# Optimization experiments

Hardware: AMD Instinct MI355X
Metric: run time of the kernel (lower is better)

Reference implementation:

```python
import jax, jax.numpy as jnp
import numpy as np

D_MODEL = 512
N_HEADS = 8
D_FF = 1024
LV = 2048
LT = 512
GAMMA = 0.9
SCALE_BASE = 512  # XPOS default scale_base


def _dup_interleave(m):
    # (L, d/2) -> (L, d) duplicating each column: [a,b] -> [a,a,b,b]
    return jnp.repeat(m, 2, axis=-1)


def _xpos(x, downscale=False):
    # XPOS rotary embedding (RetNet-style), x: (B, L, d)
    B, L, d = x.shape
    half = d // 2
    s = (jnp.arange(0, d, 2, dtype=jnp.float32) + 0.4 * d) / (1.4 * d)  # (d/2,)
    scale = s[None, :] ** (jnp.arange(L, dtype=jnp.float32)[:, None] / SCALE_BASE)  # (L, d/2)
    inv_freq = 1.0 / (10000.0 ** (jnp.arange(half, dtype=jnp.float32) / half))
    ang = jnp.arange(L, dtype=jnp.float32)[:, None] * inv_freq[None, :]  # (L, d/2)
    if downscale:
        scale = 1.0 / scale
    sin = _dup_interleave(jnp.sin(ang) * scale)[None]  # (1, L, d)
    cos = _dup_interleave(jnp.cos(ang) * scale)[None]
    x1, x2 = x[..., 0::2], x[..., 1::2]
    rot = jnp.stack((-x2, x1), axis=-1).reshape(x.shape)  # rotate_every_two
    return x * cos + rot * sin


def _sine_pos(L, d):
    # DETR-style normalized 1D sine position embedding, mask = ones(1, L)
    x_embed = jnp.arange(1, L + 1, dtype=jnp.float32)  # cumsum of ones
    x_embed = x_embed / (x_embed[-1] + 1e-6) * (2.0 * np.pi)
    dim_t = jnp.arange(d, dtype=jnp.float32)
    dim_t = 10000.0 ** (2.0 * jnp.floor(dim_t / 2.0) / d)
    pos = x_embed[:, None] / dim_t[None, :]  # (L, d)
    pos = jnp.stack((jnp.sin(pos[:, 0::2]), jnp.cos(pos[:, 1::2])), axis=2).reshape(L, d)
    return pos[None]  # (1, L, d)


def _ln(x, w, b, eps=1e-5):
    mu = jnp.mean(x, axis=-1, keepdims=True)
    var = jnp.var(x, axis=-1, keepdims=True)
    return (x - mu) / jnp.sqrt(var + eps) * w + b


def _ret_forward(src_vid, src_txt, ln1_w, ln1_b, wq, bq, wk, bk, wv, bv, wo, bo,
                 lin1_w, lin1_b, lin2_w, lin2_b, ln2_w, ln2_b, ln3_w, ln3_b,
                 learn_ret_w):
    B, Lv, D = src_vid.shape
    Lt = src_txt.shape[1]
    h, dk = N_HEADS, D // N_HEADS

    # retention decay matrix D[n,m] = gamma^(n-m) for n>=m else 0
    n = jnp.arange(Lv)
    delta = jnp.maximum(n[:, None] - n[None, :], 0).astype(jnp.float32)
    Dm = jnp.where(n[:, None] >= n[None, :], GAMMA ** delta, 0.0)

    # learned sparse mask
    learn = jax.nn.sigmoid(learn_ret_w.reshape(Lv, Lv))
    diag = jnp.eye(Lv, dtype=jnp.float32)
    video_ret = (1.0 - diag) * learn
    learn_mask = diag + video_ret
    mask = Dm * learn_mask  # mask_choice == 'both'
    loss_sparsity = jnp.mean(jnp.abs(video_ret))

    # position encodings
    pos_vid_q = _xpos(src_vid)
    pos_vid_k = _xpos(src_vid, downscale=True)
    pos_txt = _sine_pos(Lt, D)
    src = jnp.concatenate([src_vid, src_txt], axis=1)       # (B, Lv+Lt, D)
    pos = jnp.concatenate([pos_vid_q, pos_txt], axis=1)
    pos_k = jnp.concatenate([pos_vid_k, pos_txt], axis=1)

    # --- RetLayer (eval mode: dropout = identity) ---
    src2 = _ln(src, ln1_w, ln1_b)
    q = src2[:, :Lv] + pos[:, :Lv]
    k = src2[:, :Lv] + pos_k[:, :Lv]
    v = src2[:, :Lv]

    # multi-head attention with MULTIPLICATIVE mask on logits
    qh = (q @ wq.T + bq).reshape(B, Lv, h, dk) / jnp.sqrt(jnp.float32(dk))
    kh = (k @ wk.T + bk).reshape(B, Lv, h, dk)
    vh = (v @ wv.T + bv).reshape(B, Lv, h, dk)
    attn = jnp.einsum('blhd,bmhd->bhlm', qh, kh) * mask[None, None]
    attn = jax.nn.softmax(attn, axis=-1)
    vid_att = jnp.einsum('bhlm,bmhd->blhd', attn, vh).reshape(B, Lv, D)
    vid_att = vid_att @ wo.T + bo

    src2 = jnp.concatenate([vid_att, src2[:, Lv:]], axis=1) + pos
    src = src + src2
    src2 = _ln(src, ln2_w, ln2_b)
    src2 = jax.nn.gelu(src2 @ lin1_w.T + lin1_b, approximate=False) @ lin2_w.T + lin2_b
    src = src + src2
    src = _ln(src, ln3_w, ln3_b)
    return src[:, :Lv], src[:, Lv:], loss_sparsity


def setup_inputs() -> dict:
    key = jax.random.key(0)
    ks = jax.random.split(key, 12)
    D, F = D_MODEL, D_FF
    w = lambda k, shp: (jax.random.normal(k, shp, dtype=jnp.float32) * 0.02)
    return {
        'src_vid': jax.random.normal(ks[0], (1, LV, D), dtype=jnp.float32),
        'src_txt': jax.random.normal(ks[1], (1, LT, D), dtype=jnp.float32),
        'ln1_w': jnp.ones((D,), jnp.float32), 'ln1_b': jnp.zeros((D,), jnp.float32),
        'wq': w(ks[2], (D, D)), 'bq': jnp.zeros((D,), jnp.float32),
        'wk': w(ks[3], (D, D)), 'bk': jnp.zeros((D,), jnp.float32),
        'wv': w(ks[4], (D, D)), 'bv': jnp.zeros((D,), jnp.float32),
        'wo': w(ks[5], (D, D)), 'bo': jnp.zeros((D,), jnp.float32),
        'lin1_w': w(ks[6], (F, D)), 'lin1_b': jnp.zeros((F,), jnp.float32),
        'lin2_w': w(ks[7], (D, F)), 'lin2_b': jnp.zeros((D,), jnp.float32),
        'ln2_w': jnp.ones((D,), jnp.float32), 'ln2_b': jnp.zeros((D,), jnp.float32),
        'ln3_w': jnp.ones((D,), jnp.float32), 'ln3_b': jnp.zeros((D,), jnp.float32),
        'learn_ret_w': jax.random.normal(ks[8], (LV * LV,), dtype=jnp.float32),
    }


def reference(src_vid, src_txt, ln1_w, ln1_b, wq, bq, wk, bk, wv, bv, wo, bo,
              lin1_w, lin1_b, lin2_w, lin2_b, ln2_w, ln2_b, ln3_w, ln3_b,
              learn_ret_w):
    return _ret_forward(src_vid, src_txt, ln1_w, ln1_b, wq, bq, wk, bk, wv, bv,
                        wo, bo, lin1_w, lin1_b, lin2_w, lin2_b, ln2_w, ln2_b,
                        ln3_w, ln3_b, learn_ret_w)
```

## Files before the change

kernel.cpp:

```cpp
#include <hip/hip_runtime.h>
#include <hip/hip_bf16.h>
#include <math.h>

#define LVID 2048
#define LTXT 512
#define DMOD 512
#define LTOT 2560
#define LOG2_GAMMA (-0.15200309344504995f)
#define LOG2E 1.4426950408889634f

typedef __bf16 bf16x8 __attribute__((ext_vector_type(8)));
typedef float f32x4 __attribute__((ext_vector_type(4)));

__device__ inline f32x4 mfma_bf16(bf16x8 a, bf16x8 b, f32x4 c) {
  return __builtin_amdgcn_mfma_f32_16x16x32_bf16(a, b, c, 0, 0, 0);
}

__device__ inline void gload_lds16(const void* g, void* l) {
  __builtin_amdgcn_global_load_lds(
      (const __attribute__((address_space(1))) void*)g,
      (__attribute__((address_space(3))) void*)l, 16, 0, 0);
}

union U8 { __hip_bfloat16 b[8]; uint4 u; };

__global__ __launch_bounds__(256) void k_prep_ln1(
    const float* __restrict__ lw, float* __restrict__ premask2,
    float* __restrict__ lossp, float* __restrict__ vts,
    const float* __restrict__ wq, const float* __restrict__ wk,
    const float* __restrict__ wv, const float* __restrict__ wo,
    const float* __restrict__ l1, const float* __restrict__ l2,
    __hip_bfloat16* __restrict__ dst,
    const float* __restrict__ src_vid, const float* __restrict__ src_txt,
    const float* __restrict__ w, const float* __restrict__ b,
    __hip_bfloat16* __restrict__ acat, float* __restrict__ srcA,
    float* __restrict__ posb) {
  int tid = threadIdx.x;
  int blk = blockIdx.x;
  if (blk < 64) vts[blk * 256 + tid] = 0.f;
  if (blk < 2048) {
    __shared__ float red[256];
    int i = blk;
    int i0r = i & ~63;
    int tloCol = (i0r > 900) ? (((i0r - 900) >> 6) << 6) : 0;
    int idx0 = (blk * 256 + tid) * 8;
    int j0 = idx0 & 2047;
    float4 lv0 = *(const float4*)&lw[idx0];
    float4 lv1 = *(const float4*)&lw[idx0 + 4];
    float lvv[8] = {lv0.x, lv0.y, lv0.z, lv0.w, lv1.x, lv1.y, lv1.z, lv1.w};
    float pm[8];
    float s = 0.f;
#pragma unroll
    for (int e = 0; e < 8; e++) {
      int j = j0 + e;
      float sig = 1.f / (1.f + __expf(-lvv[e]));
      if (j != i) s += sig;
      float m = (j > i) ? 0.f
              : ((j == i) ? 1.f : exp2f((float)(i - j) * LOG2_GAMMA) * sig);
      pm[e] = m * LOG2E;
    }
    if (j0 >= tloCol && j0 < i0r + 64) {
      *(float4*)&premask2[idx0]     = *(float4*)&pm[0];
      *(float4*)&premask2[idx0 + 4] = *(float4*)&pm[4];
    }
    red[tid] = s; __syncthreads();
    for (int st = 128; st > 0; st >>= 1) { if (tid < st) red[tid] += red[tid + st]; __syncthreads(); }
    if (tid == 0) lossp[blk] = red[0];
  } else if (blk < 4096) {
    int i4 = (blk - 2048) * 256 + tid;
    const float* sp; int base;
    if (i4 < 131072)      { if (i4 < 65536)  { sp = wq; base = 0; }      else { sp = wk; base = 65536; } }
    else if (i4 < 262144) { if (i4 < 196608) { sp = wv; base = 131072; } else { sp = wo; base = 196608; } }
    else if (i4 < 393216) { sp = l1; base = 262144; }
    else                  { sp = l2; base = 393216; }
    float4 v = ((const float4*)sp)[i4 - base];
    __hip_bfloat16 o[4] = {__float2bfloat16(v.x), __float2bfloat16(v.y),
                           __float2bfloat16(v.z), __float2bfloat16(v.w)};
    *(uint2*)(dst + (size_t)i4 * 4) = *(uint2*)o;
  } else {
    int row = (blk - 4096) * 4 + (tid >> 6);
    int lane = tid & 63;
    const float* xs = (row < LVID) ? (src_vid + (size_t)row * DMOD)
                                   : (src_txt + (size_t)(row - LVID) * DMOD);
    float x[8];
    { float4 v0 = *(const float4*)&xs[lane * 8];
      float4 v1 = *(const float4*)&xs[lane * 8 + 4];
      x[0]=v0.x; x[1]=v0.y; x[2]=v0.z; x[3]=v0.w;
      x[4]=v1.x; x[5]=v1.y; x[6]=v1.z; x[7]=v1.w; }
    float s = 0.f;
#pragma unroll
    for (int i = 0; i < 8; i++) s += x[i];
#pragma unroll
    for (int st = 1; st < 64; st <<= 1) s += __shfl_xor(s, st, 64);
    float mu = s * (1.f / DMOD);
    float vs = 0.f;
#pragma unroll
    for (int i = 0; i < 8; i++) { float d = x[i] - mu; vs += d * d; }
#pragma unroll
    for (int st = 1; st < 64; st <<= 1) vs += __shfl_xor(vs, st, 64);
    float inv = rsqrtf(vs * (1.f / DMOD) + 1e-5f);
    float y[8];
    { float4 w0 = *(const float4*)&w[lane * 8];
      float4 w1 = *(const float4*)&w[lane * 8 + 4];
      float4 b0 = *(const float4*)&b[lane * 8];
      float4 b1 = *(const float4*)&b[lane * 8 + 4];
      float wv_[8] = {w0.x,w0.y,w0.z,w0.w,w1.x,w1.y,w1.z,w1.w};
      float bv_[8] = {b0.x,b0.y,b0.z,b0.w,b1.x,b1.y,b1.z,b1.w};
#pragma unroll
      for (int i = 0; i < 8; i++) y[i] = (x[i] - mu) * inv * wv_[i] + bv_[i]; }
    size_t base = (size_t)row * DMOD + lane * 8;
    if (row < LVID) {
      U8 pv;
#pragma unroll
      for (int i = 0; i < 8; i++) pv.b[i] = __float2bfloat16(y[i]);
      *(uint4*)&acat[(size_t)(4096 + row) * DMOD + lane * 8] = pv.u;
      float pq[8], pk[8];
      float l = (float)row;
#pragma unroll
      for (int p = 0; p < 4; p++) {
        int j = lane * 4 + p;
        float sj = (2.f * j + 204.8f) * (1.f / 716.8f);
        float scale = __powf(sj, l * (1.f / 512.f));
        float invfreq = __powf(10000.f, -(float)j * (1.f / 256.f));
        float sn, cs; __sincosf(l * invfreq, &sn, &cs);
        float cq = cs * scale, sq = sn * scale;
        pq[2*p]   = x[2*p] * cq - x[2*p+1] * sq;
        pq[2*p+1] = x[2*p+1] * cq + x[2*p] * sq;
        float isc = 1.f / scale;
        float ck = cs * isc, sk = sn * isc;
        pk[2*p]   = x[2*p] * ck - x[2*p+1] * sk;
        pk[2*p+1] = x[2*p+1] * ck + x[2*p] * sk;
      }
      *(float4*)&posb[base]     = *(float4*)&pq[0];
      *(float4*)&posb[base + 4] = *(float4*)&pq[4];
      U8 pqv, pkv;
#pragma unroll
      for (int i = 0; i < 8; i++) {
        pqv.b[i] = __float2bfloat16(y[i] + pq[i]);
        pkv.b[i] = __float2bfloat16(y[i] + pk[i]);
      }
      *(uint4*)&acat[(size_t)row * DMOD + lane * 8] = pqv.u;
      *(uint4*)&acat[(size_t)(2048 + row) * DMOD + lane * 8] = pkv.u;
    } else {
      int l = row - LVID;
      float xe = (float)(l + 1) * (6.28318530717958647692f / 512.000001f);
      float o8[8];
#pragma unroll
      for (int p = 0; p < 4; p++) {
        int j = lane * 4 + p;
        float dimt = __powf(10000.f, (float)j * (1.f / 256.f));
        float a = xe / dimt;
        o8[2*p]   = x[2*p]   + y[2*p]   + __sinf(a);
        o8[2*p+1] = x[2*p+1] + y[2*p+1] + __cosf(a);
      }
      *(float4*)&srcA[base]     = *(float4*)&o8[0];
      *(float4*)&srcA[base + 4] = *(float4*)&o8[4];
    }
  }
}

__global__ __launch_bounds__(256) void k_ln2(
    const float* __restrict__ srcA,
    const float* __restrict__ w, const float* __restrict__ b,
    __hip_bfloat16* __restrict__ obf) {
  int row = blockIdx.x * 4 + (threadIdx.x >> 6);
  int lane = threadIdx.x & 63;
  size_t base = (size_t)row * DMOD + lane * 8;
  float x[8];
  { float4 v0 = *(const float4*)&srcA[base];
    float4 v1 = *(const float4*)&srcA[base + 4];
    x[0]=v0.x; x[1]=v0.y; x[2]=v0.z; x[3]=v0.w;
    x[4]=v1.x; x[5]=v1.y; x[6]=v1.z; x[7]=v1.w; }
  float s = 0.f;
#pragma unroll
  for (int i = 0; i < 8; i++) s += x[i];
#pragma unroll
  for (int st = 1; st < 64; st <<= 1) s += __shfl_xor(s, st, 64);
  float mu = s * (1.f / DMOD);
  float vs = 0.f;
#pragma unroll
  for (int i = 0; i < 8; i++) { float d = x[i] - mu; vs += d * d; }
#pragma unroll
  for (int st = 1; st < 64; st <<= 1) vs += __shfl_xor(vs, st, 64);
  float inv = rsqrtf(vs * (1.f / DMOD) + 1e-5f);
  float4 w0 = *(const float4*)&w[lane * 8];
  float4 w1 = *(const float4*)&w[lane * 8 + 4];
  float4 b0 = *(const float4*)&b[lane * 8];
  float4 b1 = *(const float4*)&b[lane * 8 + 4];
  float wv_[8] = {w0.x,w0.y,w0.z,w0.w,w1.x,w1.y,w1.z,w1.w};
  float bv_[8] = {b0.x,b0.y,b0.z,b0.w,b1.x,b1.y,b1.z,b1.w};
  U8 o;
#pragma unroll
  for (int i = 0; i < 8; i++)
    o.b[i] = __float2bfloat16((x[i] - mu) * inv * wv_[i] + bv_[i]);
  *(uint4*)&obf[base] = o.u;
}

__global__ __launch_bounds__(256) void k_ln3(
    const float* __restrict__ srcA, const float* __restrict__ ffo0,
    const float* __restrict__ ffo1,
    const float* __restrict__ w, const float* __restrict__ b,
    float* __restrict__ o, const float* __restrict__ lossp) {
  if (blockIdx.x == 0 && threadIdx.x < 64) {
    float s = 0.f;
    for (int i = threadIdx.x; i < 2048; i += 64) s += lossp[i];
#pragma unroll
    for (int st = 1; st < 64; st <<= 1) s += __shfl_xor(s, st, 64);
    if (threadIdx.x == 0) o[1310720] = s * (1.f / 4194304.f);
  }
  int row = blockIdx.x * 4 + (threadIdx.x >> 6);
  int lane = threadIdx.x & 63;
  size_t base = (size_t)row * DMOD + lane * 8;
  float x[8];
  { float4 a0 = *(const float4*)&srcA[base];
    float4 a1 = *(const float4*)&srcA[base + 4];
    float4 f0 = *(const float4*)&ffo0[base];
    float4 f1 = *(const float4*)&ffo0[base + 4];
    float4 g0 = *(const float4*)&ffo1[base];
    float4 g1 = *(const float4*)&ffo1[base + 4];
    x[0]=a0.x+f0.x+g0.x; x[1]=a0.y+f0.y+g0.y; x[2]=a0.z+f0.z+g0.z; x[3]=a0.w+f0.w+g0.w;
    x[4]=a1.x+f1.x+g1.x; x[5]=a1.y+f1.y+g1.y; x[6]=a1.z+f1.z+g1.z; x[7]=a1.w+f1.w+g1.w; }
  float s = 0.f;
#pragma unroll
  for (int i = 0; i < 8; i++) s += x[i];
#pragma unroll
  for (int st = 1; st < 64; st <<= 1) s += __shfl_xor(s, st, 64);
  float mu = s * (1.f / DMOD);
  float vs = 0.f;
#pragma unroll
  for (int i = 0; i < 8; i++) { float d = x[i] - mu; vs += d * d; }
#pragma unroll
  for (int st = 1; st < 64; st <<= 1) vs += __shfl_xor(vs, st, 64);
  float inv = rsqrtf(vs * (1.f / DMOD) + 1e-5f);
  float4 w0 = *(const float4*)&w[lane * 8];
  float4 w1 = *(const float4*)&w[lane * 8 + 4];
  float4 b0 = *(const float4*)&b[lane * 8];
  float4 b1 = *(const float4*)&b[lane * 8 + 4];
  float wv_[8] = {w0.x,w0.y,w0.z,w0.w,w1.x,w1.y,w1.z,w1.w};
  float bv_[8] = {b0.x,b0.y,b0.z,b0.w,b1.x,b1.y,b1.z,b1.w};
  float y[8];
#pragma unroll
  for (int i = 0; i < 8; i++) y[i] = (x[i] - mu) * inv * wv_[i] + bv_[i];
  *(float4*)&o[base]     = *(float4*)&y[0];
  *(float4*)&o[base + 4] = *(float4*)&y[4];
}

template <int EPI>
__global__ __launch_bounds__(256) void k_gemm5(
    const __hip_bfloat16* __restrict__ A, const __hip_bfloat16* __restrict__ W0,
    const float* __restrict__ b0, const float* __restrict__ b1,
    const float* __restrict__ b2, void* __restrict__ Cv,
    const float* __restrict__ res1, const float* __restrict__ res2,
    __hip_bfloat16* __restrict__ vT, float* __restrict__ vts,
    int M, int N, int K) {
  __shared__ __hip_bfloat16 sA[2][4096];
  __shared__ __hip_bfloat16 sB[2][4096];
  int tid = threadIdx.x, lane = tid & 63, w = tid >> 6;
  int c16 = lane & 15, q4 = lane >> 4;
  int bm = blockIdx.y * 64, bn = blockIdx.x * 64;
  int seg = (EPI == 3) ? (bm >> 11) : 0;
  const __hip_bfloat16* Wp = (EPI == 3) ? (W0 + (size_t)seg * ((size_t)N * K)) : W0;
  int kb   = (EPI == 5) ? (int)blockIdx.z * (K >> 1) : 0;
  int Keff = (EPI == 5) ? (K >> 1) : K;
  int r0 = tid >> 2, cc0 = (tid & 3) * 8;
  const __hip_bfloat16* gA = A  + (size_t)(bm + r0) * K + kb + cc0;
  const __hip_bfloat16* gB = Wp + (size_t)(bn + r0) * K + kb + cc0;
  auto stage = [&](int buf, int k0) {
    gload_lds16(gA + k0,      &sA[buf][(size_t)tid * 8]);
    gload_lds16(gA + k0 + 32, &sA[buf][2048 + (size_t)tid * 8]);
    gload_lds16(gB + k0,      &sB[buf][(size_t)tid * 8]);
    gload_lds16(gB + k0 + 32, &sB[buf][2048 + (size_t)tid * 8]);
  };
  f32x4 acc[2][2];
  { f32x4 z = {0.f,0.f,0.f,0.f}; acc[0][0]=z; acc[0][1]=z; acc[1][0]=z; acc[1][1]=z; }
  int wm = w & 1, wn = w >> 1;
  const int S = Keff >> 6;
  stage(0, 0);
  for (int s = 0; s < S; s++) {
    __syncthreads();
    if (s + 1 < S) stage((s + 1) & 1, (s + 1) * 64);
    int bf = s & 1;
#pragma unroll
    for (int kc = 0; kc < 2; kc++) {
      bf16x8 a0  = *(const bf16x8*)&sA[bf][kc*2048 + (wm*32 + c16) * 32 + q4*8];
      bf16x8 a1  = *(const bf16x8*)&sA[bf][kc*2048 + (wm*32 + 16 + c16) * 32 + q4*8];
      bf16x8 bv0 = *(const bf16x8*)&sB[bf][kc*2048 + (wn*32 + c16) * 32 + q4*8];
      bf16x8 bv1 = *(const bf16x8*)&sB[bf][kc*2048 + (wn*32 + 16 + c16) * 32 + q4*8];
      acc[0][0] = mfma_bf16(a0, bv0, acc[0][0]);
      acc[0][1] = mfma_bf16(a0, bv1, acc[0][1]);
      acc[1][0] = mfma_bf16(a1, bv0, acc[1][0]);
      acc[1][1] = mfma_bf16(a1, bv1, acc[1][1]);
    }
  }
  float alpha = (EPI == 3 && seg == 0) ? 0.125f : 1.f;
  const float* bp = (EPI == 3) ? (seg == 0 ? b0 : (seg == 1 ? b1 : b2)) : b0;
  if (EPI == 3 && seg == 2) {
    int tile = (bm & 2047) >> 6;
    float vsum[2] = {0.f, 0.f};
#pragma unroll
    for (int j = 0; j < 2; j++) {
      int n = bn + wn*32 + j*16 + c16;
      float bs = bp[n];
#pragma unroll
      for (int i = 0; i < 2; i++) {
        ushort4 u; float vv[4];
#pragma unroll
        for (int r = 0; r < 4; r++) {
          __hip_bfloat16 vb = __float2bfloat16(acc[i][j][r] + bs);
          ((__hip_bfloat16*)&u)[r] = vb;
          vv[r] = __bfloat162float(vb);
        }
        int jj = (bm & 2047) + wm*32 + i*16 + q4*4;
        *(ushort4*)&vT[(size_t)n * 2048 + jj] = u;
        vsum[j] += vv[0] + vv[1] + vv[2] + vv[3];
      }
    }
#pragma unroll
    for (int j = 0; j < 2; j++) {
      float s2 = vsum[j];
      s2 += __shfl_xor(s2, 16, 64);
      s2 += __shfl_xor(s2, 32, 64);
      int n = bn + wn*32 + j*16 + c16;
      if (q4 == 0) atomicAdd(&vts[(size_t)(n >> 6) * 2048 + tile * 64 + (n & 63)], s2);
    }
    return;
  }
#pragma unroll
  for (int j = 0; j < 2; j++) {
    int n = bn + wn*32 + j*16 + c16;
    float bs = bp[n];
    if (EPI == 5 && blockIdx.z != 0) bs = 0.f;
#pragma unroll
    for (int i = 0; i < 2; i++) {
#pragma unroll
      for (int r = 0; r < 4; r++) {
        int m = bm + wm*32 + i*16 + q4*4 + r;
        float v = (acc[i][j][r] + bs) * alpha;
        if (EPI == 4) v = 0.5f * v * (1.f + erff(v * 0.70710678118654752f));
        if (EPI == 2) {
          size_t off = (size_t)m * N + n;
          ((float*)Cv)[off] = v + res1[off] + res2[off];
        } else if (EPI == 4) {
          ((__hip_bfloat16*)Cv)[(size_t)m * N + n] = __float2bfloat16(v);
        } else if (EPI == 5) {
          ((float*)Cv)[(size_t)blockIdx.z * 1310720 + (size_t)m * N + n] = v;
        } else {
          ((__hip_bfloat16*)Cv)[(size_t)(m & 2047) * 1024 + seg * 512 + n] = __float2bfloat16(v);
        }
      }
    }
  }
}

__global__ __launch_bounds__(256) void k_attn(
    const __hip_bfloat16* __restrict__ qkb,
    const float* __restrict__ premask2,
    const __hip_bfloat16* __restrict__ vT,
    __hip_bfloat16* __restrict__ Obuf,
    float* __restrict__ ml) {
  __shared__ __hip_bfloat16 sQ[64][72];
  __shared__ __hip_bfloat16 sK[2][64][72];
  __shared__ __hip_bfloat16 sVt[2][64][72];
  __shared__ __hip_bfloat16 sP[64][72];
  int i0 = blockIdx.x * 64, h = blockIdx.y, z = blockIdx.z;
  int tid = threadIdx.x, lane = tid & 63, w = tid >> 6;
  int c16 = lane & 15, q4 = lane >> 4;
  {
    int r = tid >> 2, c0 = (tid & 3) * 16;
    const __hip_bfloat16* g = qkb + (size_t)(i0 + r) * 1024 + h * 64 + c0;
    *(uint4*)&sQ[r][c0]     = *(const uint4*)g;
    *(uint4*)&sQ[r][c0 + 8] = *(const uint4*)(g + 8);
  }
  int thi = i0 >> 6;
  int tlo = (i0 > 900) ? ((i0 - 900) >> 6) : 0;
  int nt_ = thi - tlo + 1;
  int t0 = tlo + ((nt_ * z) >> 2);
  int t1 = tlo + ((nt_ * (z + 1)) >> 2) - 1;
  float rm = 0.f, rz = 0.f;
  f32x4 O[4];
  { f32x4 zz = {0.f,0.f,0.f,0.f}; O[0]=zz; O[1]=zz; O[2]=zz; O[3]=zz; }
  int kr = tid >> 2, kc = (tid & 3) * 16;
  uint4 pk0, pk1, pv0, pv1;
  if (t0 <= t1) {
    const __hip_bfloat16* gk = qkb + (size_t)(t0*64 + kr) * 1024 + 512 + h*64 + kc;
    pk0 = *(const uint4*)gk; pk1 = *(const uint4*)(gk + 8);
    const __hip_bfloat16* gv = vT + (size_t)(h*64 + kr) * 2048 + t0*64 + kc;
    pv0 = *(const uint4*)gv; pv1 = *(const uint4*)(gv + 8);
  }
  for (int t = t0; t <= t1; t++) {
    int buf = (t - t0) & 1;
    *(uint4*)&sK[buf][kr][kc]      = pk0;
    *(uint4*)&sK[buf][kr][kc + 8]  = pk1;
    *(uint4*)&sVt[buf][kr][kc]     = pv0;
    *(uint4*)&sVt[buf][kr][kc + 8] = pv1;
    __syncthreads();
    if (t < t1) {
      const __hip_bfloat16* gk = qkb + (size_t)((t+1)*64 + kr) * 1024 + 512 + h*64 + kc;
      pk0 = *(const uint4*)gk; pk1 = *(const uint4*)(gk + 8);
      const __hip_bfloat16* gv = vT + (size_t)(h*64 + kr) * 2048 + (t+1)*64 + kc;
      pv0 = *(const uint4*)gv; pv1 = *(const uint4*)(gv + 8);
    }
    bf16x8 bq0 = *(const bf16x8*)&sQ[w*16 + c16][q4*8];
    bf16x8 bq1 = *(const bf16x8*)&sQ[w*16 + c16][32 + q4*8];
    f32x4 St[4];
#pragma unroll
    for (int jt = 0; jt < 4; jt++) {
      f32x4 zz = {0.f,0.f,0.f,0.f};
      bf16x8 a0 = *(const bf16x8*)&sK[buf][jt*16 + c16][q4*8];
      bf16x8 a1 = *(const bf16x8*)&sK[buf][jt*16 + c16][32 + q4*8];
      zz = mfma_bf16(a0, bq0, zz);
      zz = mfma_bf16(a1, bq1, zz);
      St[jt] = zz;
    }
    int qg = i0 + w*16 + c16;
    float lg[4][4];
    float tmax = -3.0e38f;
#pragma unroll
    for (int jt = 0; jt < 4; jt++) {
      float4 pm = *(const float4*)&premask2[(size_t)qg * 2048 + t*64 + jt*16 + q4*4];
      lg[jt][0] = St[jt][0] * pm.x; lg[jt][1] = St[jt][1] * pm.y;
      lg[jt][2] = St[jt][2] * pm.z; lg[jt][3] = St[jt][3] * pm.w;
#pragma unroll
      for (int r = 0; r < 4; r++) tmax = fmaxf(tmax, lg[jt][r]);
    }
    tmax = fmaxf(tmax, __shfl_xor(tmax, 16, 64));
    tmax = fmaxf(tmax, __shfl_xor(tmax, 32, 64));
    float mn = fmaxf(rm, tmax);
    float al = exp2f(rm - mn);
    rm = mn;
    float zp = 0.f;
#pragma unroll
    for (int jt = 0; jt < 4; jt++) {
      U8 e4;
      float e0 = exp2f(lg[jt][0] - rm), e1 = exp2f(lg[jt][1] - rm);
      float e2 = exp2f(lg[jt][2] - rm), e3 = exp2f(lg[jt][3] - rm);
      zp += e0 + e1 + e2 + e3;
      e4.b[0] = __float2bfloat16(e0); e4.b[1] = __float2bfloat16(e1);
      e4.b[2] = __float2bfloat16(e2); e4.b[3] = __float2bfloat16(e3);
      *(uint2*)&sP[w*16 + c16][jt*16 + q4*4] = *(uint2*)&e4.b[0];
    }
    zp += __shfl_xor(zp, 16, 64);
    zp += __shfl_xor(zp, 32, 64);
    rz = rz * al + zp;
    float alr[4];
#pragma unroll
    for (int r = 0; r < 4; r++) alr[r] = __shfl(al, q4*4 + r, 64);
#pragma unroll
    for (int dt = 0; dt < 4; dt++)
#pragma unroll
      for (int r = 0; r < 4; r++) O[dt][r] *= alr[r];
    bf16x8 ap0 = *(const bf16x8*)&sP[w*16 + c16][q4*8];
    bf16x8 ap1 = *(const bf16x8*)&sP[w*16 + c16][32 + q4*8];
#pragma unroll
    for (int dt = 0; dt < 4; dt++) {
      bf16x8 bv0 = *(const bf16x8*)&sVt[buf][dt*16 + c16][q4*8];
      bf16x8 bv1 = *(const bf16x8*)&sVt[buf][dt*16 + c16][32 + q4*8];
      O[dt] = mfma_bf16(ap0, bv0, O[dt]);
      O[dt] = mfma_bf16(ap1, bv1, O[dt]);
    }
  }
  __hip_bfloat16* ob = Obuf + (size_t)z * (2048 * 512);
#pragma unroll
  for (int dt = 0; dt < 4; dt++) {
    int d = dt*16 + c16;
#pragma unroll
    for (int r = 0; r < 4; r++)
      ob[(size_t)(i0 + w*16 + q4*4 + r) * DMOD + h*64 + d] = __float2bfloat16(O[dt][r]);
  }
  if (q4 == 0) {
    size_t mi = (((size_t)z * 8 + h) * 2048 + i0 + w*16 + c16) * 2;
    ml[mi] = rm; ml[mi + 1] = rz;
  }
}

__global__ __launch_bounds__(256) void k_comb(
    const __hip_bfloat16* __restrict__ Obuf, const float* __restrict__ ml,
    const float* __restrict__ vts,
    __hip_bfloat16* __restrict__ outp) {
  __shared__ float sV[32][64];
  __shared__ float sS[64];
  __shared__ float sC[64][6];
  int i0 = blockIdx.x * 64, h = blockIdx.y;
  int tid = threadIdx.x;
  int thi = i0 >> 6;
  int tlo = (i0 > 900) ? ((i0 - 900) >> 6) : 0;
  int n = thi - tlo + 1;
  float nu = (float)(2048 - 64 * n);
  {
    const float4* src = (const float4*)(vts + (size_t)h * 2048);
    ((float4*)&sV[0][0])[tid * 2]     = src[tid * 2];
    ((float4*)&sV[0][0])[tid * 2 + 1] = src[tid * 2 + 1];
  }
  __syncthreads();
  if (tid < 64) {
    float s = 0.f;
    for (int t = 0; t < 32; t++) if (t < tlo || t > thi) s += sV[t][tid];
    sS[tid] = s;
  } else if (tid < 128) {
    int r = tid - 64;
    int row = i0 + r;
    float m[4], l[4];
#pragma unroll
    for (int z = 0; z < 4; z++) {
      size_t mi = (((size_t)z * 8 + h) * 2048 + row) * 2;
      m[z] = ml[mi]; l[z] = ml[mi + 1];
    }
    float M = fmaxf(fmaxf(m[0], m[1]), fmaxf(m[2], m[3]));
    float au = exp2f(-M);
    float a[4], D = nu * au;
#pragma unroll
    for (int z = 0; z < 4; z++) { a[z] = exp2f(m[z] - M); D += l[z] * a[z]; }
    float dinv = 1.f / D;
#pragma unroll
    for (int z = 0; z < 4; z++) sC[r][z] = a[z] * dinv;
    sC[r][4] = au * dinv;
  }
  __syncthreads();
  int r = tid >> 2, dc = (tid & 3) * 16;
  size_t off = (size_t)(i0 + r) * DMOD + h * 64 + dc;
  float c[4];
#pragma unroll
  for (int z = 0; z < 4; z++) c[z] = sC[r][z];
  float cu = sC[r][4];
  float va[16], vb[16];
#pragma unroll
  for (int k = 0; k < 16; k++) { va[k] = sS[dc + (k & 7)] * 0.f; }
  U8 oa, obb;
#pragma unroll
  for (int k = 0; k < 8; k++) { va[k] = sS[dc + k] * cu; vb[k] = sS[dc + 8 + k] * cu; }
#pragma unroll
  for (int z = 0; z < 4; z++) {
    U8 pa, pb;
    pa.u = *(const uint4*)&Obuf[(size_t)z * 2048 * 512 + off];
    pb.u = *(const uint4*)&Obuf[(size_t)z * 2048 * 512 + off + 8];
#pragma unroll
    for (int k = 0; k < 8; k++) {
      va[k] += __bfloat162float(pa.b[k]) * c[z];
      vb[k] += __bfloat162float(pb.b[k]) * c[z];
    }
  }
#pragma unroll
  for (int k = 0; k < 8; k++) {
    oa.b[k]  = __float2bfloat16(va[k]);
    obb.b[k] = __float2bfloat16(vb[k]);
  }
  *(uint4*)&outp[off]     = oa.u;
  *(uint4*)&outp[off + 8] = obb.u;
}

extern "C" void kernel_launch(void* const* d_in, const int* in_sizes, int n_in,
                              void* d_out, int out_size, void* d_ws, size_t ws_size,
                              hipStream_t stream) {
  const float* src_vid = (const float*)d_in[0];
  const float* src_txt = (const float*)d_in[1];
  const float* ln1_w = (const float*)d_in[2];
  const float* ln1_b = (const float*)d_in[3];
  const float* wq = (const float*)d_in[4];
  const float* bq = (const float*)d_in[5];
  const float* wk = (const float*)d_in[6];
  const float* bk = (const float*)d_in[7];
  const float* wv = (const float*)d_in[8];
  const float* bv = (const float*)d_in[9];
  const float* wo = (const float*)d_in[10];
  const float* bo = (const float*)d_in[11];
  const float* lin1_w = (const float*)d_in[12];
  const float* lin1_b = (const float*)d_in[13];
  const float* lin2_w = (const float*)d_in[14];
  const float* lin2_b = (const float*)d_in[15];
  const float* ln2_w = (const float*)d_in[16];
  const float* ln2_b = (const float*)d_in[17];
  const float* ln3_w = (const float*)d_in[18];
  const float* ln3_b = (const float*)d_in[19];
  const float* lw = (const float*)d_in[20];
  float* out = (float*)d_out;

  const size_t MB = 1048576;
  char* wsb = (char*)d_ws;
  float* premask2       = (float*)(wsb + 0);
  __hip_bfloat16* wqb   = (__hip_bfloat16*)(wsb + 16*MB);
  __hip_bfloat16* wob   = wqb + 786432;
  __hip_bfloat16* l1b   = wqb + 1048576;
  __hip_bfloat16* l2b   = wqb + 1572864;
  __hip_bfloat16* acat  = (__hip_bfloat16*)(wsb + 20*MB);
  __hip_bfloat16* qkb   = (__hip_bfloat16*)(wsb + 26*MB);
  __hip_bfloat16* vTb   = (__hip_bfloat16*)(wsb + 30*MB);
  __hip_bfloat16* Obuf  = (__hip_bfloat16*)(wsb + 32*MB);
  float* mlb            = (float*)(wsb + 40*MB);
  float* vts            = (float*)(wsb + 41*MB);
  __hip_bfloat16* vattb = (__hip_bfloat16*)(wsb + 42*MB);
  float* srcA           = (float*)(wsb + 44*MB);
  float* posb           = (float*)(wsb + 49*MB);
  __hip_bfloat16* s2b   = (__hip_bfloat16*)(wsb + 54*MB);
  __hip_bfloat16* hidb  = (__hip_bfloat16*)(wsb + 57*MB);
  float* ffo0           = (float*)(wsb + 62*MB);
  float* ffo1           = (float*)(wsb + 67*MB);
  float* lossp          = (float*)(wsb + 72*MB);

  k_prep_ln1<<<4736, 256, 0, stream>>>(lw, premask2, lossp, vts,
      wq, wk, wv, wo, lin1_w, lin2_w, wqb,
      src_vid, src_txt, ln1_w, ln1_b, acat, srcA, posb);

  k_gemm5<3><<<dim3(8, 96), 256, 0, stream>>>(acat, wqb, bq, bk, bv,
      qkb, nullptr, nullptr, vTb, vts, 6144, 512, 512);
  k_attn<<<dim3(32, 8, 4), 256, 0, stream>>>(qkb, premask2, vTb, Obuf, mlb);
  k_comb<<<dim3(32, 8), 256, 0, stream>>>(Obuf, mlb, vts, vattb);
  k_gemm5<2><<<dim3(8, 32), 256, 0, stream>>>(vattb, wob, bo, nullptr, nullptr,
      srcA, src_vid, posb, nullptr, nullptr, 2048, 512, 512);
  k_ln2<<<640, 256, 0, stream>>>(srcA, ln2_w, ln2_b, s2b);
  k_gemm5<4><<<dim3(16, 40), 256, 0, stream>>>(s2b, l1b, lin1_b, nullptr, nullptr,
      hidb, nullptr, nullptr, nullptr, nullptr, 2560, 1024, 512);
  k_gemm5<5><<<dim3(8, 40, 2), 256, 0, stream>>>(hidb, l2b, lin2_b, nullptr, nullptr,
      ffo0, nullptr, nullptr, nullptr, nullptr, 2560, 512, 1024);
  k_ln3<<<640, 256, 0, stream>>>(srcA, ffo0, ffo1, ln3_w, ln3_b, out, lossp);
}
```

Baseline: 206.6 us.

## Compute decay mask inline in attention and use 128-row GEMM tiles

The precomputed premask buffer is removed. The attention kernel now computes gamma decay times sigmoid of the learned weights directly from the raw weights, and the prep kernel only reduces the sigmoid sum for the loss using fewer, wider blocks. Separately, a new GEMM variant with 128x64 tiles (4x2 MFMA per wave) is used for the QKV, FFN1 and FFN2 GEMMs to increase data reuse. This saves a 16MB write and read pass for the mask, at the cost of extra exp and sigmoid work inside attention and fewer GEMM blocks per launch.

```diff
diff --git a/kernel.cpp b/kernel.cpp
--- a/kernel.cpp
+++ b/kernel.cpp
@@ -25,8 +25,8 @@
 union U8 { __hip_bfloat16 b[8]; uint4 u; };
 
 __global__ __launch_bounds__(256) void k_prep_ln1(
-    const float* __restrict__ lw, float* __restrict__ premask2,
-    float* __restrict__ lossp, float* __restrict__ vts,
+    const float* __restrict__ lw, float* __restrict__ lossp,
+    float* __restrict__ vts,
     const float* __restrict__ wq, const float* __restrict__ wk,
     const float* __restrict__ wv, const float* __restrict__ wo,
     const float* __restrict__ l1, const float* __restrict__ l2,
@@ -38,36 +38,26 @@
   int tid = threadIdx.x;
   int blk = blockIdx.x;
   if (blk < 64) vts[blk * 256 + tid] = 0.f;
-  if (blk < 2048) {
+  if (blk < 512) {
     __shared__ float red[256];
-    int i = blk;
-    int i0r = i & ~63;
-    int tloCol = (i0r > 900) ? (((i0r - 900) >> 6) << 6) : 0;
-    int idx0 = (blk * 256 + tid) * 8;
-    int j0 = idx0 & 2047;
-    float4 lv0 = *(const float4*)&lw[idx0];
-    float4 lv1 = *(const float4*)&lw[idx0 + 4];
-    float lvv[8] = {lv0.x, lv0.y, lv0.z, lv0.w, lv1.x, lv1.y, lv1.z, lv1.w};
-    float pm[8];
+    int idx0 = blk * 8192 + tid * 32;
+    int i = idx0 >> 11, j0 = idx0 & 2047;
     float s = 0.f;
 #pragma unroll
-    for (int e = 0; e < 8; e++) {
-      int j = j0 + e;
-      float sig = 1.f / (1.f + __expf(-lvv[e]));
-      if (j != i) s += sig;
-      float m = (j > i) ? 0.f
-              : ((j == i) ? 1.f : exp2f((float)(i - j) * LOG2_GAMMA) * sig);
-      pm[e] = m * LOG2E;
-    }
-    if (j0 >= tloCol && j0 < i0r + 64) {
-      *(float4*)&premask2[idx0]     = *(float4*)&pm[0];
-      *(float4*)&premask2[idx0 + 4] = *(float4*)&pm[4];
+    for (int g = 0; g < 8; g++) {
+      float4 a = *(const float4*)&lw[idx0 + g * 4];
+      float av[4] = {a.x, a.y, a.z, a.w};
+#pragma unroll
+      for (int c = 0; c < 4; c++) {
+        int j = j0 + g * 4 + c;
+        if (j != i) s += 1.f / (1.f + __expf(-av[c]));
+      }
     }
     red[tid] = s; __syncthreads();
     for (int st = 128; st > 0; st >>= 1) { if (tid < st) red[tid] += red[tid + st]; __syncthreads(); }
     if (tid == 0) lossp[blk] = red[0];
-  } else if (blk < 4096) {
-    int i4 = (blk - 2048) * 256 + tid;
+  } else if (blk < 2560) {
+    int i4 = (blk - 512) * 256 + tid;
     const float* sp; int base;
     if (i4 < 131072)      { if (i4 < 65536)  { sp = wq; base = 0; }      else { sp = wk; base = 65536; } }
     else if (i4 < 262144) { if (i4 < 196608) { sp = wv; base = 131072; } else { sp = wo; base = 196608; } }
@@ -78,7 +68,7 @@
                            __float2bfloat16(v.z), __float2bfloat16(v.w)};
     *(uint2*)(dst + (size_t)i4 * 4) = *(uint2*)o;
   } else {
-    int row = (blk - 4096) * 4 + (tid >> 6);
+    int row = (blk - 2560) * 4 + (tid >> 6);
     int lane = tid & 63;
     const float* xs = (row < LVID) ? (src_vid + (size_t)row * DMOD)
                                    : (src_txt + (size_t)(row - LVID) * DMOD);
@@ -203,7 +193,7 @@
     float* __restrict__ o, const float* __restrict__ lossp) {
   if (blockIdx.x == 0 && threadIdx.x < 64) {
     float s = 0.f;
-    for (int i = threadIdx.x; i < 2048; i += 64) s += lossp[i];
+    for (int i = threadIdx.x; i < 512; i += 64) s += lossp[i];
 #pragma unroll
     for (int st = 1; st < 64; st <<= 1) s += __shfl_xor(s, st, 64);
     if (threadIdx.x == 0) o[1310720] = s * (1.f / 4194304.f);
@@ -248,23 +238,17 @@
 template <int EPI>
 __global__ __launch_bounds__(256) void k_gemm5(
     const __hip_bfloat16* __restrict__ A, const __hip_bfloat16* __restrict__ W0,
-    const float* __restrict__ b0, const float* __restrict__ b1,
-    const float* __restrict__ b2, void* __restrict__ Cv,
+    const float* __restrict__ b0, void* __restrict__ Cv,
     const float* __restrict__ res1, const float* __restrict__ res2,
-    __hip_bfloat16* __restrict__ vT, float* __restrict__ vts,
     int M, int N, int K) {
   __shared__ __hip_bfloat16 sA[2][4096];
   __shared__ __hip_bfloat16 sB[2][4096];
   int tid = threadIdx.x, lane = tid & 63, w = tid >> 6;
   int c16 = lane & 15, q4 = lane >> 4;
   int bm = blockIdx.y * 64, bn = blockIdx.x * 64;
-  int seg = (EPI == 3) ? (bm >> 11) : 0;
-  const __hip_bfloat16* Wp = (EPI == 3) ? (W0 + (size_t)seg * ((size_t)N * K)) : W0;
-  int kb   = (EPI == 5) ? (int)blockIdx.z * (K >> 1) : 0;
-  int Keff = (EPI == 5) ? (K >> 1) : K;
   int r0 = tid >> 2, cc0 = (tid & 3) * 8;
-  const __hip_bfloat16* gA = A  + (size_t)(bm + r0) * K + kb + cc0;
-  const __hip_bfloat16* gB = Wp + (size_t)(bn + r0) * K + kb + cc0;
+  const __hip_bfloat16* gA = A  + (size_t)(bm + r0) * K + cc0;
+  const __hip_bfloat16* gB = W0 + (size_t)(bn + r0) * K + cc0;
   auto stage = [&](int buf, int k0) {
     gload_lds16(gA + k0,      &sA[buf][(size_t)tid * 8]);
     gload_lds16(gA + k0 + 32, &sA[buf][2048 + (size_t)tid * 8]);
@@ -274,7 +258,7 @@
   f32x4 acc[2][2];
   { f32x4 z = {0.f,0.f,0.f,0.f}; acc[0][0]=z; acc[0][1]=z; acc[1][0]=z; acc[1][1]=z; }
   int wm = w & 1, wn = w >> 1;
-  const int S = Keff >> 6;
+  const int S = K >> 6;
   stage(0, 0);
   for (int s = 0; s < S; s++) {
     __syncthreads();
@@ -292,27 +276,97 @@
       acc[1][1] = mfma_bf16(a1, bv1, acc[1][1]);
     }
   }
+#pragma unroll
+  for (int j = 0; j < 2; j++) {
+    int n = bn + wn*32 + j*16 + c16;
+    float bs = b0[n];
+#pragma unroll
+    for (int i = 0; i < 2; i++) {
+#pragma unroll
+      for (int r = 0; r < 4; r++) {
+        int m = bm + wm*32 + i*16 + q4*4 + r;
+        float v = acc[i][j][r] + bs;
+        size_t off = (size_t)m * N + n;
+        ((float*)Cv)[off] = v + res1[off] + res2[off];
+      }
+    }
+  }
+}
+
+template <int EPI>
+__global__ __launch_bounds__(256) void k_gemm6(
+    const __hip_bfloat16* __restrict__ A, const __hip_bfloat16* __restrict__ W0,
+    const float* __restrict__ b0, const float* __restrict__ b1,
+    const float* __restrict__ b2, void* __restrict__ Cv,
+    __hip_bfloat16* __restrict__ vT, float* __restrict__ vts,
+    int M, int N, int K) {
+  __shared__ __hip_bfloat16 sA[2][8192];
+  __shared__ __hip_bfloat16 sB[2][4096];
+  int tid = threadIdx.x, lane = tid & 63, w = tid >> 6;
+  int c16 = lane & 15, q4 = lane >> 4;
+  int bm = blockIdx.y * 128, bn = blockIdx.x * 64;
+  int seg = (EPI == 3) ? (bm >> 11) : 0;
+  const __hip_bfloat16* Wp = (EPI == 3) ? (W0 + (size_t)seg * ((size_t)N * K)) : W0;
+  int kb   = (EPI == 5) ? (int)blockIdx.z * (K >> 1) : 0;
+  int Keff = (EPI == 5) ? (K >> 1) : K;
+  int r0 = tid >> 2, cc0 = (tid & 3) * 8;
+  const __hip_bfloat16* gA = A  + (size_t)(bm + r0) * K + kb + cc0;
+  const __hip_bfloat16* gB = Wp + (size_t)(bn + r0) * K + kb + cc0;
+  auto stage = [&](int buf, int k0) {
+    gload_lds16(gA + k0,                    &sA[buf][(size_t)tid * 8]);
+    gload_lds16(gA + (size_t)64 * K + k0,   &sA[buf][2048 + (size_t)tid * 8]);
+    gload_lds16(gA + k0 + 32,               &sA[buf][4096 + (size_t)tid * 8]);
+    gload_lds16(gA + (size_t)64 * K + k0+32,&sA[buf][6144 + (size_t)tid * 8]);
+    gload_lds16(gB + k0,                    &sB[buf][(size_t)tid * 8]);
+    gload_lds16(gB + k0 + 32,               &sB[buf][2048 + (size_t)tid * 8]);
+  };
+  f32x4 acc[4][2];
+  { f32x4 z = {0.f,0.f,0.f,0.f};
+#pragma unroll
+    for (int i = 0; i < 4; i++) { acc[i][0] = z; acc[i][1] = z; } }
+  int wm = w & 1, wn = w >> 1;
+  const int S = Keff >> 6;
+  stage(0, 0);
+  for (int s = 0; s < S; s++) {
+    __syncthreads();
+    if (s + 1 < S) stage((s + 1) & 1, (s + 1) * 64);
+    int bf = s & 1;
+#pragma unroll
+    for (int kc = 0; kc < 2; kc++) {
+      bf16x8 av[4], bvv[2];
+#pragma unroll
+      for (int i = 0; i < 4; i++)
+        av[i] = *(const bf16x8*)&sA[bf][kc*4096 + (wm*64 + i*16 + c16) * 32 + q4*8];
+#pragma unroll
+      for (int j = 0; j < 2; j++)
+        bvv[j] = *(const bf16x8*)&sB[bf][kc*2048 + (wn*32 + j*16 + c16) * 32 + q4*8];
+#pragma unroll
+      for (int i = 0; i < 4; i++)
+#pragma unroll
+        for (int j = 0; j < 2; j++)
+          acc[i][j] = mfma_bf16(av[i], bvv[j], acc[i][j]);
+    }
+  }
   float alpha = (EPI == 3 && seg == 0) ? 0.125f : 1.f;
   const float* bp = (EPI == 3) ? (seg == 0 ? b0 : (seg == 1 ? b1 : b2)) : b0;
   if (EPI == 3 && seg == 2) {
-    int tile = (bm & 2047) >> 6;
+    int tile = ((bm & 2047) + wm * 64) >> 6;
     float vsum[2] = {0.f, 0.f};
 #pragma unroll
     for (int j = 0; j < 2; j++) {
       int n = bn + wn*32 + j*16 + c16;
       float bs = bp[n];
 #pragma unroll
-      for (int i = 0; i < 2; i++) {
-        ushort4 u; float vv[4];
+      for (int i = 0; i < 4; i++) {
+        ushort4 u;
 #pragma unroll
         for (int r = 0; r < 4; r++) {
           __hip_bfloat16 vb = __float2bfloat16(acc[i][j][r] + bs);
           ((__hip_bfloat16*)&u)[r] = vb;
-          vv[r] = __bfloat162float(vb);
+          vsum[j] += __bfloat162float(vb);
         }
-        int jj = (bm & 2047) + wm*32 + i*16 + q4*4;
+        int jj = (bm & 2047) + wm*64 + i*16 + q4*4;
         *(ushort4*)&vT[(size_t)n * 2048 + jj] = u;
-        vsum[j] += vv[0] + vv[1] + vv[2] + vv[3];
       }
     }
 #pragma unroll
@@ -331,16 +385,13 @@
     float bs = bp[n];
     if (EPI == 5 && blockIdx.z != 0) bs = 0.f;
 #pragma unroll
-    for (int i = 0; i < 2; i++) {
+    for (int i = 0; i < 4; i++) {
 #pragma unroll
       for (int r = 0; r < 4; r++) {
-        int m = bm + wm*32 + i*16 + q4*4 + r;
+        int m = bm + wm*64 + i*16 + q4*4 + r;
         float v = (acc[i][j][r] + bs) * alpha;
-        if (EPI == 4) v = 0.5f * v * (1.f + erff(v * 0.70710678118654752f));
-        if (EPI == 2) {
-          size_t off = (size_t)m * N + n;
-          ((float*)Cv)[off] = v + res1[off] + res2[off];
-        } else if (EPI == 4) {
+        if (EPI == 4) {
+          v = 0.5f * v * (1.f + erff(v * 0.70710678118654752f));
           ((__hip_bfloat16*)Cv)[(size_t)m * N + n] = __float2bfloat16(v);
         } else if (EPI == 5) {
           ((float*)Cv)[(size_t)blockIdx.z * 1310720 + (size_t)m * N + n] = v;
@@ -354,7 +405,7 @@
 
 __global__ __launch_bounds__(256) void k_attn(
     const __hip_bfloat16* __restrict__ qkb,
-    const float* __restrict__ premask2,
+    const float* __restrict__ lw,
     const __hip_bfloat16* __restrict__ vT,
     __hip_bfloat16* __restrict__ Obuf,
     float* __restrict__ ml) {
@@ -413,15 +464,25 @@
       St[jt] = zz;
     }
     int qg = i0 + w*16 + c16;
+    const float* lwrow = lw + (size_t)qg * 2048 + t*64;
     float lg[4][4];
     float tmax = -3.0e38f;
 #pragma unroll
     for (int jt = 0; jt < 4; jt++) {
-      float4 pm = *(const float4*)&premask2[(size_t)qg * 2048 + t*64 + jt*16 + q4*4];
-      lg[jt][0] = St[jt][0] * pm.x; lg[jt][1] = St[jt][1] * pm.y;
-      lg[jt][2] = St[jt][2] * pm.z; lg[jt][3] = St[jt][3] * pm.w;
-#pragma unroll
-      for (int r = 0; r < 4; r++) tmax = fmaxf(tmax, lg[jt][r]);
+      int jb = jt*16 + q4*4;
+      float4 lv4 = *(const float4*)&lwrow[jb];
+      float lv[4] = {lv4.x, lv4.y, lv4.z, lv4.w};
+#pragma unroll
+      for (int r = 0; r < 4; r++) {
+        int d = qg - (t*64 + jb + r);
+        float pm;
+        if (d < 0)       pm = 0.f;
+        else if (d == 0) pm = LOG2E;
+        else pm = (exp2f((float)d * LOG2_GAMMA) * (1.f / (1.f + __expf(-lv[r])))) * LOG2E;
+        float v = St[jt][r] * pm;
+        lg[jt][r] = v;
+        tmax = fmaxf(tmax, v);
+      }
     }
     tmax = fmaxf(tmax, __shfl_xor(tmax, 16, 64));
     tmax = fmaxf(tmax, __shfl_xor(tmax, 32, 64));
@@ -522,10 +583,7 @@
 #pragma unroll
   for (int z = 0; z < 4; z++) c[z] = sC[r][z];
   float cu = sC[r][4];
-  float va[16], vb[16];
-#pragma unroll
-  for (int k = 0; k < 16; k++) { va[k] = sS[dc + (k & 7)] * 0.f; }
-  U8 oa, obb;
+  float va[8], vb[8];
 #pragma unroll
   for (int k = 0; k < 8; k++) { va[k] = sS[dc + k] * cu; vb[k] = sS[dc + 8 + k] * cu; }
 #pragma unroll
@@ -539,6 +597,7 @@
       vb[k] += __bfloat162float(pb.b[k]) * c[z];
     }
   }
+  U8 oa, obb;
 #pragma unroll
   for (int k = 0; k < 8; k++) {
     oa.b[k]  = __float2bfloat16(va[k]);
@@ -576,7 +635,6 @@
 
   const size_t MB = 1048576;
   char* wsb = (char*)d_ws;
-  float* premask2       = (float*)(wsb + 0);
   __hip_bfloat16* wqb   = (__hip_bfloat16*)(wsb + 16*MB);
   __hip_bfloat16* wob   = wqb + 786432;
   __hip_bfloat16* l1b   = wqb + 1048576;
@@ -596,20 +654,20 @@
   float* ffo1           = (float*)(wsb + 67*MB);
   float* lossp          = (float*)(wsb + 72*MB);
 
-  k_prep_ln1<<<4736, 256, 0, stream>>>(lw, premask2, lossp, vts,
+  k_prep_ln1<<<3200, 256, 0, stream>>>(lw, lossp, vts,
       wq, wk, wv, wo, lin1_w, lin2_w, wqb,
       src_vid, src_txt, ln1_w, ln1_b, acat, srcA, posb);
 
-  k_gemm5<3><<<dim3(8, 96), 256, 0, stream>>>(acat, wqb, bq, bk, bv,
-      qkb, nullptr, nullptr, vTb, vts, 6144, 512, 512);
-  k_attn<<<dim3(32, 8, 4), 256, 0, stream>>>(qkb, premask2, vTb, Obuf, mlb);
+  k_gemm6<3><<<dim3(8, 48), 256, 0, stream>>>(acat, wqb, bq, bk, bv,
+      qkb, vTb, vts, 6144, 512, 512);
+  k_attn<<<dim3(32, 8, 4), 256, 0, stream>>>(qkb, lw, vTb, Obuf, mlb);
   k_comb<<<dim3(32, 8), 256, 0, stream>>>(Obuf, mlb, vts, vattb);
-  k_gemm5<2><<<dim3(8, 32), 256, 0, stream>>>(vattb, wob, bo, nullptr, nullptr,
-      srcA, src_vid, posb, nullptr, nullptr, 2048, 512, 512);
+  k_gemm5<2><<<dim3(8, 32), 256, 0, stream>>>(vattb, wob, bo,
+      srcA, src_vid, posb, 2048, 512, 512);
   k_ln2<<<640, 256, 0, stream>>>(srcA, ln2_w, ln2_b, s2b);
-  k_gemm5<4><<<dim3(16, 40), 256, 0, stream>>>(s2b, l1b, lin1_b, nullptr, nullptr,
-      hidb, nullptr, nullptr, nullptr, nullptr, 2560, 1024, 512);
-  k_gemm5<5><<<dim3(8, 40, 2), 256, 0, stream>>>(hidb, l2b, lin2_b, nullptr, nullptr,
-      ffo0, nullptr, nullptr, nullptr, nullptr, 2560, 512, 1024);
+  k_gemm6<4><<<dim3(16, 20), 256, 0, stream>>>(s2b, l1b, lin1_b, nullptr, nullptr,
+      hidb, nullptr, nullptr, 2560, 1024, 512);
+  k_gemm6<5><<<dim3(8, 20, 2), 256, 0, stream>>>(hidb, l2b, lin2_b, nullptr, nullptr,
+      ffo0, nullptr, nullptr, 2560, 512, 1024);
   k_ln3<<<640, 256, 0, stream>>>(srcA, ffo0, ffo1, ln3_w, ln3_b, out, lossp);
 }
```

Measured after the change: 221.0 us. 6.9% more time.

## Stage GEMM K dimension in two large LDS phases instead of double-buffered steps

Applied to the files above, without the earlier changes.

The bf16 MFMA GEMM now loads half of the K=512 reduction (256 columns of A and B) into LDS in one burst, then runs 8 MFMA k-steps. It repeats this once, replacing the eight double-buffered 64-wide stages. The aim is to put many more global-to-LDS loads in flight and cut the number of barriers. The cost is that loads and compute no longer overlap within a phase, and the 64KB of LDS per block lowers occupancy. The code now assumes the effective K is always 512. Dead temporaries in the V-sum epilogue and the combine kernel are also removed.

```diff
diff --git a/kernel.cpp b/kernel.cpp
--- a/kernel.cpp
+++ b/kernel.cpp
@@ -246,46 +246,42 @@
 }
 
 template <int EPI>
-__global__ __launch_bounds__(256) void k_gemm5(
+__global__ __launch_bounds__(256) void k_gemm8(
     const __hip_bfloat16* __restrict__ A, const __hip_bfloat16* __restrict__ W0,
     const float* __restrict__ b0, const float* __restrict__ b1,
     const float* __restrict__ b2, void* __restrict__ Cv,
     const float* __restrict__ res1, const float* __restrict__ res2,
     __hip_bfloat16* __restrict__ vT, float* __restrict__ vts,
     int M, int N, int K) {
-  __shared__ __hip_bfloat16 sA[2][4096];
-  __shared__ __hip_bfloat16 sB[2][4096];
+  __shared__ __hip_bfloat16 sA[16384];
+  __shared__ __hip_bfloat16 sB[16384];
   int tid = threadIdx.x, lane = tid & 63, w = tid >> 6;
   int c16 = lane & 15, q4 = lane >> 4;
   int bm = blockIdx.y * 64, bn = blockIdx.x * 64;
   int seg = (EPI == 3) ? (bm >> 11) : 0;
   const __hip_bfloat16* Wp = (EPI == 3) ? (W0 + (size_t)seg * ((size_t)N * K)) : W0;
-  int kb   = (EPI == 5) ? (int)blockIdx.z * (K >> 1) : 0;
-  int Keff = (EPI == 5) ? (K >> 1) : K;
+  int kb = (EPI == 5) ? (int)blockIdx.z * (K >> 1) : 0;
   int r0 = tid >> 2, cc0 = (tid & 3) * 8;
   const __hip_bfloat16* gA = A  + (size_t)(bm + r0) * K + kb + cc0;
   const __hip_bfloat16* gB = Wp + (size_t)(bn + r0) * K + kb + cc0;
-  auto stage = [&](int buf, int k0) {
-    gload_lds16(gA + k0,      &sA[buf][(size_t)tid * 8]);
-    gload_lds16(gA + k0 + 32, &sA[buf][2048 + (size_t)tid * 8]);
-    gload_lds16(gB + k0,      &sB[buf][(size_t)tid * 8]);
-    gload_lds16(gB + k0 + 32, &sB[buf][2048 + (size_t)tid * 8]);
-  };
   f32x4 acc[2][2];
   { f32x4 z = {0.f,0.f,0.f,0.f}; acc[0][0]=z; acc[0][1]=z; acc[1][0]=z; acc[1][1]=z; }
   int wm = w & 1, wn = w >> 1;
-  const int S = Keff >> 6;
-  stage(0, 0);
-  for (int s = 0; s < S; s++) {
+#pragma unroll
+  for (int ph = 0; ph < 2; ph++) {
+    if (ph) __syncthreads();
+#pragma unroll
+    for (int g = 0; g < 8; g++) {
+      gload_lds16(gA + ph * 256 + g * 32, &sA[g * 2048 + (size_t)tid * 8]);
+      gload_lds16(gB + ph * 256 + g * 32, &sB[g * 2048 + (size_t)tid * 8]);
+    }
     __syncthreads();
-    if (s + 1 < S) stage((s + 1) & 1, (s + 1) * 64);
-    int bf = s & 1;
-#pragma unroll
-    for (int kc = 0; kc < 2; kc++) {
-      bf16x8 a0  = *(const bf16x8*)&sA[bf][kc*2048 + (wm*32 + c16) * 32 + q4*8];
-      bf16x8 a1  = *(const bf16x8*)&sA[bf][kc*2048 + (wm*32 + 16 + c16) * 32 + q4*8];
-      bf16x8 bv0 = *(const bf16x8*)&sB[bf][kc*2048 + (wn*32 + c16) * 32 + q4*8];
-      bf16x8 bv1 = *(const bf16x8*)&sB[bf][kc*2048 + (wn*32 + 16 + c16) * 32 + q4*8];
+#pragma unroll
+    for (int kk = 0; kk < 8; kk++) {
+      bf16x8 a0  = *(const bf16x8*)&sA[kk*2048 + (wm*32 + c16) * 32 + q4*8];
+      bf16x8 a1  = *(const bf16x8*)&sA[kk*2048 + (wm*32 + 16 + c16) * 32 + q4*8];
+      bf16x8 bv0 = *(const bf16x8*)&sB[kk*2048 + (wn*32 + c16) * 32 + q4*8];
+      bf16x8 bv1 = *(const bf16x8*)&sB[kk*2048 + (wn*32 + 16 + c16) * 32 + q4*8];
       acc[0][0] = mfma_bf16(a0, bv0, acc[0][0]);
       acc[0][1] = mfma_bf16(a0, bv1, acc[0][1]);
       acc[1][0] = mfma_bf16(a1, bv0, acc[1][0]);
@@ -303,16 +299,15 @@
       float bs = bp[n];
 #pragma unroll
       for (int i = 0; i < 2; i++) {
-        ushort4 u; float vv[4];
+        ushort4 u;
 #pragma unroll
         for (int r = 0; r < 4; r++) {
           __hip_bfloat16 vb = __float2bfloat16(acc[i][j][r] + bs);
           ((__hip_bfloat16*)&u)[r] = vb;
-          vv[r] = __bfloat162float(vb);
+          vsum[j] += __bfloat162float(vb);
         }
         int jj = (bm & 2047) + wm*32 + i*16 + q4*4;
         *(ushort4*)&vT[(size_t)n * 2048 + jj] = u;
-        vsum[j] += vv[0] + vv[1] + vv[2] + vv[3];
       }
     }
 #pragma unroll
@@ -336,12 +331,12 @@
       for (int r = 0; r < 4; r++) {
         int m = bm + wm*32 + i*16 + q4*4 + r;
         float v = (acc[i][j][r] + bs) * alpha;
-        if (EPI == 4) v = 0.5f * v * (1.f + erff(v * 0.70710678118654752f));
-        if (EPI == 2) {
+        if (EPI == 4) {
+          v = 0.5f * v * (1.f + erff(v * 0.70710678118654752f));
+          ((__hip_bfloat16*)Cv)[(size_t)m * N + n] = __float2bfloat16(v);
+        } else if (EPI == 2) {
           size_t off = (size_t)m * N + n;
           ((float*)Cv)[off] = v + res1[off] + res2[off];
-        } else if (EPI == 4) {
-          ((__hip_bfloat16*)Cv)[(size_t)m * N + n] = __float2bfloat16(v);
         } else if (EPI == 5) {
           ((float*)Cv)[(size_t)blockIdx.z * 1310720 + (size_t)m * N + n] = v;
         } else {
@@ -522,10 +517,7 @@
 #pragma unroll
   for (int z = 0; z < 4; z++) c[z] = sC[r][z];
   float cu = sC[r][4];
-  float va[16], vb[16];
-#pragma unroll
-  for (int k = 0; k < 16; k++) { va[k] = sS[dc + (k & 7)] * 0.f; }
-  U8 oa, obb;
+  float va[8], vb[8];
 #pragma unroll
   for (int k = 0; k < 8; k++) { va[k] = sS[dc + k] * cu; vb[k] = sS[dc + 8 + k] * cu; }
 #pragma unroll
@@ -539,6 +531,7 @@
       vb[k] += __bfloat162float(pb.b[k]) * c[z];
     }
   }
+  U8 oa, obb;
 #pragma unroll
   for (int k = 0; k < 8; k++) {
     oa.b[k]  = __float2bfloat16(va[k]);
@@ -600,16 +593,16 @@
       wq, wk, wv, wo, lin1_w, lin2_w, wqb,
       src_vid, src_txt, ln1_w, ln1_b, acat, srcA, posb);
 
-  k_gemm5<3><<<dim3(8, 96), 256, 0, stream>>>(acat, wqb, bq, bk, bv,
+  k_gemm8<3><<<dim3(8, 96), 256, 0, stream>>>(acat, wqb, bq, bk, bv,
       qkb, nullptr, nullptr, vTb, vts, 6144, 512, 512);
   k_attn<<<dim3(32, 8, 4), 256, 0, stream>>>(qkb, premask2, vTb, Obuf, mlb);
   k_comb<<<dim3(32, 8), 256, 0, stream>>>(Obuf, mlb, vts, vattb);
-  k_gemm5<2><<<dim3(8, 32), 256, 0, stream>>>(vattb, wob, bo, nullptr, nullptr,
+  k_gemm8<2><<<dim3(8, 32), 256, 0, stream>>>(vattb, wob, bo, nullptr, nullptr,
       srcA, src_vid, posb, nullptr, nullptr, 2048, 512, 512);
   k_ln2<<<640, 256, 0, stream>>>(srcA, ln2_w, ln2_b, s2b);
-  k_gemm5<4><<<dim3(16, 40), 256, 0, stream>>>(s2b, l1b, lin1_b, nullptr, nullptr,
+  k_gemm8<4><<<dim3(16, 40), 256, 0, stream>>>(s2b, l1b, lin1_b, nullptr, nullptr,
       hidb, nullptr, nullptr, nullptr, nullptr, 2560, 1024, 512);
-  k_gemm5<5><<<dim3(8, 40, 2), 256, 0, stream>>>(hidb, l2b, lin2_b, nullptr, nullptr,
+  k_gemm8<5><<<dim3(8, 40, 2), 256, 0, stream>>>(hidb, l2b, lin2_b, nullptr, nullptr,
       ffo0, nullptr, nullptr, nullptr, nullptr, 2560, 512, 1024);
   k_ln3<<<640, 256, 0, stream>>>(srcA, ffo0, ffo1, ln3_w, ln3_b, out, lossp);
 }
```

Result: slower. 213.1 us (+3.1%).
